# Optimization experiments

Hardware: AMD Instinct MI355X
Metric: run time of the kernel (lower is better)

Reference implementation:

```python
import jax, jax.numpy as jnp
import numpy as np

N = 4096
F = 1024
UNITS = 128
HEADS = 8
MASK_VAL = -10000000000.0  # -1e10, matches the source
LEAKY_ALPHA = 0.2


def setup_inputs() -> dict:
    key = jax.random.key(0)
    ks = jax.random.split(key, 6)
    X = jax.random.normal(ks[0], (1, N, F), dtype=jnp.float32)
    # Binary adjacency with self-loops (the layer expects self-loops preprocessed in).
    u = jax.random.uniform(ks[1], (N, N), dtype=jnp.float32)
    A = ((u < 0.01).astype(jnp.float32) + jnp.eye(N, dtype=jnp.float32))
    A = jnp.minimum(A, 1.0)[None]  # [1, N, N]
    W = jax.random.normal(ks[2], (HEADS, F, UNITS), dtype=jnp.float32) * (1.0 / np.sqrt(F))
    a_self = jax.random.normal(ks[3], (HEADS, UNITS), dtype=jnp.float32) * 0.1
    a_neigh = jax.random.normal(ks[4], (HEADS, UNITS), dtype=jnp.float32) * 0.1
    b = jnp.zeros((HEADS, UNITS), dtype=jnp.float32)
    return {"X": X, "A": A, "W": W, "a_self": a_self, "a_neigh": a_neigh, "b": b}


def reference(X, A, W, a_self, a_neigh, b):
    x = X[0]   # [N, F]
    adj = A[0]  # [N, N]
    # Per-head feature projection: [H, N, U]
    feat = jnp.einsum("nf,hfu->hnu", x, W)
    # Additive attention logits: e_ij = leaky_relu(a_s . h_i + a_n . h_j)
    s = jnp.einsum("hnu,hu->hn", feat, a_self)    # [H, N]
    t = jnp.einsum("hnu,hu->hn", feat, a_neigh)   # [H, N]
    dense = s[:, :, None] + t[:, None, :]          # [H, N, N]
    dense = jax.nn.leaky_relu(dense, negative_slope=LEAKY_ALPHA)
    # Mask non-edges with -1e10 (dense += -1e10 * (1 - A))
    dense = dense + MASK_VAL * (1.0 - adj)[None]
    attn = jax.nn.softmax(dense, axis=-1)          # [H, N, N]
    # Weighted aggregation + bias: [H, N, U]
    h = jnp.einsum("hnm,hmu->hnu", attn, feat) + b[:, None, :]
    # Concat heads: [N, H*U]
    out = jnp.transpose(h, (1, 0, 2)).reshape(N, HEADS * UNITS)
    out = jax.nn.relu(out)
    return out[None]  # [1, N, H*U]
```

## Files before the change

### kernel.cpp

```cpp
#include <hip/hip_runtime.h>


constexpr int NN = 4096;
constexpr int FF = 1024;
constexpr int HH = 8;
constexpr int UU = 128;
constexpr int CC = HH * UU;
constexpr int MAXDEG = 128;
constexpr float ALPHA = 0.2f;

typedef __attribute__((ext_vector_type(8))) short short8;
typedef __attribute__((ext_vector_type(4))) float f32x4;

__device__ inline unsigned short f2bf(float x) {
  unsigned u = __float_as_uint(x);
  return (unsigned short)((u + 0x7fffu + ((u >> 16) & 1u)) >> 16);
}
__device__ inline float bf2f(unsigned short h) { return __uint_as_float(((unsigned)h) << 16); }

__global__ __launch_bounds__(256) void transposeW(const float* __restrict__ W,
                                                  unsigned short* __restrict__ WT) {
  const int h = blockIdx.x >> 3, ft = blockIdx.x & 7;
  const int f0 = ft * 128;
  __shared__ unsigned short hiT[128][136];
  __shared__ unsigned short loT[128][136];
  const int tid = threadIdx.x;
#pragma unroll
  for (int it = 0; it < 16; ++it) {
    int idx = it * 256 + tid;
    int r = idx >> 5;
    int u4 = idx & 31;
    float4 v = *(const float4*)(W + (size_t)h * FF * UU + (size_t)(f0 + r) * UU + u4 * 4);
    float xs[4] = {v.x, v.y, v.z, v.w};
#pragma unroll
    for (int e = 0; e < 4; ++e) {
      unsigned short hb = f2bf(xs[e]);
      hiT[u4 * 4 + e][r] = hb;
      loT[u4 * 4 + e][r] = f2bf(xs[e] - bf2f(hb));
    }
  }
  __syncthreads();
#pragma unroll
  for (int it = 0; it < 8; ++it) {
    int idx = it * 256 + tid;
    int u = idx >> 4, f8 = idx & 15;
    short8 vh = *(const short8*)&hiT[u][f8 * 8];
    short8 vl = *(const short8*)&loT[u][f8 * 8];
    size_t o = (size_t)h * UU * FF + (size_t)u * FF + f0 + f8 * 8;
    *(short8*)(WT + o) = vh;
    *(short8*)(WT + (size_t)HH * UU * FF + o) = vl;
  }
}

__global__ __launch_bounds__(256) void prep(const float* __restrict__ X,
                                            unsigned short* __restrict__ Xhi,
                                            unsigned short* __restrict__ Xlo,
                                            const float* __restrict__ A,
                                            int* __restrict__ deg,
                                            int* __restrict__ idx) {
  const int tid = threadIdx.x;
  if (blockIdx.x < 2048) {
    size_t base = ((size_t)blockIdx.x * 256 + tid) * 8;
    float4 v0 = *(const float4*)(X + base);
    float4 v1 = *(const float4*)(X + base + 4);
    float xs[8] = {v0.x, v0.y, v0.z, v0.w, v1.x, v1.y, v1.z, v1.w};
    short8 vh, vl;
#pragma unroll
    for (int e = 0; e < 8; ++e) {
      unsigned short hb = f2bf(xs[e]);
      vh[e] = (short)hb;
      vl[e] = (short)f2bf(xs[e] - bf2f(hb));
    }
    *(short8*)(Xhi + base) = vh;
    *(short8*)(Xlo + base) = vl;
    return;
  }
  const int i = blockIdx.x - 2048;
  const int lane = tid & 63;
  __shared__ int cnt;
  if (tid == 0) cnt = 0;
  __syncthreads();
  const float4* row = reinterpret_cast<const float4*>(A + (size_t)i * NN);
  for (int c = tid; c < NN / 4; c += 256) {
    float4 v = row[c];
    unsigned long long m0 = __ballot(v.x > 0.5f);
    unsigned long long m1 = __ballot(v.y > 0.5f);
    unsigned long long m2 = __ballot(v.z > 0.5f);
    unsigned long long m3 = __ballot(v.w > 0.5f);
    int wtot = __popcll(m0) + __popcll(m1) + __popcll(m2) + __popcll(m3);
    if (wtot) {
      int base = 0;
      if (lane == 0) base = atomicAdd(&cnt, wtot);
      base = __shfl(base, 0);
      unsigned long long lt = (1ull << lane) - 1;
      int c0 = __popcll(m0), c1 = __popcll(m1), c2 = __popcll(m2);
      int o;
      o = base + __popcll(m0 & lt);
      if (v.x > 0.5f && o < MAXDEG) idx[i * MAXDEG + o] = c * 4 + 0;
      o = base + c0 + __popcll(m1 & lt);
      if (v.y > 0.5f && o < MAXDEG) idx[i * MAXDEG + o] = c * 4 + 1;
      o = base + c0 + c1 + __popcll(m2 & lt);
      if (v.z > 0.5f && o < MAXDEG) idx[i * MAXDEG + o] = c * 4 + 2;
      o = base + c0 + c1 + c2 + __popcll(m3 & lt);
      if (v.w > 0.5f && o < MAXDEG) idx[i * MAXDEG + o] = c * 4 + 3;
    }
  }
  __syncthreads();
  if (tid == 0) deg[i] = cnt > MAXDEG ? MAXDEG : cnt;
}

constexpr int NTILE = 48;

__global__ __launch_bounds__(512) void gemm_mfma(const unsigned short* __restrict__ Xhi,
                                                 const unsigned short* __restrict__ Xlo,
                                                 const unsigned short* __restrict__ WT,
                                                 const float* __restrict__ a_self,
                                                 const float* __restrict__ a_neigh,
                                                 float* __restrict__ featH,
                                                 float* __restrict__ s_arr,
                                                 float* __restrict__ t_arr) {
  __shared__ char lds[2][32768];
  const int tid = threadIdx.x;
  const int w = tid >> 6, l = tid & 63;
  const int h = blockIdx.x >> 5;
  const int row0 = (blockIdx.x & 31) * 128;
  const int wr = w >> 2, wc = w & 3;

  const int lr = l >> 3;
  const int sk = ((l & 7) ^ lr) * 8;
  const unsigned short* WTh = WT + (size_t)h * UU * FF;

  f32x4 acc[4][2] = {};

  auto stage = [&](int t, int buf) {
    int s = t >> 4, kt = t & 15;
    const unsigned short* As = ((s == 1) ? Xlo : Xhi) +
        (size_t)(row0 + w * 16 + lr) * FF + kt * 64 + sk;
    const unsigned short* Bs = WTh + ((s == 2) ? (size_t)HH * UU * FF : (size_t)0) +
        (size_t)(w * 16 + lr) * FF + kt * 64 + sk;
    char* la = &lds[buf][w * 2048];
    char* lb = &lds[buf][16384 + w * 2048];
#pragma unroll
    for (int dr = 0; dr < 2; ++dr) {
      __builtin_amdgcn_global_load_lds(
          (const __attribute__((address_space(1))) unsigned int*)(As + (size_t)dr * 8 * FF),
          (__attribute__((address_space(3))) unsigned int*)(la + dr * 1024), 16, 0, 0);
      __builtin_amdgcn_global_load_lds(
          (const __attribute__((address_space(1))) unsigned int*)(Bs + (size_t)dr * 8 * FF),
          (__attribute__((address_space(3))) unsigned int*)(lb + dr * 1024), 16, 0, 0);
    }
  };

  const int arow = wr * 64 + (l & 15);
  const int bcol = wc * 32 + (l & 15);
  const int kswz = (l & 7) << 4;
  const int kb = (l >> 4) * 16;

  auto compute = [&](int buf) {
#pragma unroll
    for (int ks = 0; ks < 2; ++ks) {
      const int ko = ks * 64 + kb;
      short8 a[4], b[2];
#pragma unroll
      for (int mi = 0; mi < 4; ++mi)
        a[mi] = *(const short8*)(&lds[buf][(arow + mi * 16) * 128 + (ko ^ kswz)]);
#pragma unroll
      for (int ni = 0; ni < 2; ++ni)
        b[ni] = *(const short8*)(&lds[buf][16384 + (bcol + ni * 16) * 128 + (ko ^ kswz)]);
#pragma unroll
      for (int mi = 0; mi < 4; ++mi)
#pragma unroll
        for (int ni = 0; ni < 2; ++ni)
          acc[mi][ni] = __builtin_amdgcn_mfma_f32_16x16x32_bf16(a[mi], b[ni],
                                                                acc[mi][ni], 0, 0, 0);
    }
  };

  stage(0, 0);
  __syncthreads();
  for (int tt = 0; tt < NTILE; ++tt) {
    if (tt + 1 < NTILE) stage(tt + 1, (tt + 1) & 1);
    compute(tt & 1);
    __syncthreads();
  }

  float* fh = featH + (size_t)h * NN * UU;
  const int cu = wc * 32 + (l & 15);
  const int crow0 = row0 + wr * 64 + (l >> 4) * 4;
#pragma unroll
  for (int mi = 0; mi < 4; ++mi)
#pragma unroll
    for (int ni = 0; ni < 2; ++ni)
#pragma unroll
      for (int r = 0; r < 4; ++r)
        fh[(size_t)(crow0 + mi * 16 + r) * UU + cu + ni * 16] = acc[mi][ni][r];

  const float as0 = a_self[h * UU + cu], as1 = a_self[h * UU + cu + 16];
  const float an0 = a_neigh[h * UU + cu], an1 = a_neigh[h * UU + cu + 16];
  float ps[16], pt[16];
#pragma unroll
  for (int mi = 0; mi < 4; ++mi)
#pragma unroll
    for (int r = 0; r < 4; ++r) {
      ps[mi * 4 + r] = acc[mi][0][r] * as0 + acc[mi][1][r] * as1;
      pt[mi * 4 + r] = acc[mi][0][r] * an0 + acc[mi][1][r] * an1;
    }
#pragma unroll
  for (int mask = 1; mask <= 8; mask <<= 1)
#pragma unroll
    for (int q = 0; q < 16; ++q) {
      ps[q] += __shfl_xor(ps[q], mask);
      pt[q] += __shfl_xor(pt[q], mask);
    }
  float(*sred)[4] = (float(*)[4]) & lds[0][0];
  float(*tred)[4] = (float(*)[4]) & lds[0][2048];
  if ((l & 15) == 0) {
#pragma unroll
    for (int mi = 0; mi < 4; ++mi)
#pragma unroll
      for (int r = 0; r < 4; ++r) {
        int rl = wr * 64 + mi * 16 + (l >> 4) * 4 + r;
        sred[rl][wc] = ps[mi * 4 + r];
        tred[rl][wc] = pt[mi * 4 + r];
      }
  }
  __syncthreads();
  if (tid < 128) {
    float sv = sred[tid][0] + sred[tid][1] + sred[tid][2] + sred[tid][3];
    float tv = tred[tid][0] + tred[tid][1] + tred[tid][2] + tred[tid][3];
    s_arr[h * NN + row0 + tid] = sv;
    t_arr[h * NN + row0 + tid] = tv;
  }
}

__global__ __launch_bounds__(256) void aggregate(const float* __restrict__ featH,
                                                 const float* __restrict__ s_arr,
                                                 const float* __restrict__ t_arr,
                                                 const int* __restrict__ deg_arr,
                                                 const int* __restrict__ idx_arr,
                                                 const float* __restrict__ bias,
                                                 float* __restrict__ out) {
  const int b = blockIdx.x;
  const int h = b >> 9;
  const int i = ((b & 511) << 3) + (threadIdx.x >> 5);
  const int s32 = threadIdx.x & 31;
  const int slot = threadIdx.x >> 5;
  __shared__ int jj[8][MAXDEG];
  __shared__ float p[8][MAXDEG];

  const int deg = deg_arr[i];
  const float si = s_arr[h * NN + i];
  float e[4];
#pragma unroll
  for (int c = 0; c < 4; ++c) {
    int k = s32 + c * 32;
    int j = (k < deg) ? idx_arr[i * MAXDEG + k] : 0;
    if (k < deg) jj[slot][k] = j;
    if (k < deg) {
      float x = si + t_arr[h * NN + j];
      e[c] = x > 0.0f ? x : ALPHA * x;
    } else {
      e[c] = -3e38f;
    }
  }
  float m = fmaxf(fmaxf(e[0], e[1]), fmaxf(e[2], e[3]));
#pragma unroll
  for (int mask = 1; mask <= 16; mask <<= 1) m = fmaxf(m, __shfl_xor(m, mask));
  float pv[4], sum = 0.0f;
#pragma unroll
  for (int c = 0; c < 4; ++c) {
    pv[c] = __expf(e[c] - m);
    sum += pv[c];
  }
#pragma unroll
  for (int mask = 1; mask <= 16; mask <<= 1) sum += __shfl_xor(sum, mask);
  const float inv = 1.0f / sum;
#pragma unroll
  for (int c = 0; c < 4; ++c) p[slot][s32 + c * 32] = pv[c];

  const float* fb = featH + (size_t)h * NN * UU + s32 * 4;
  float ax = 0.0f, ay = 0.0f, az = 0.0f, aw = 0.0f;
  int k = 0;
  for (; k + 3 < deg; k += 4) {
    int j0 = jj[slot][k], j1 = jj[slot][k + 1];
    int j2 = jj[slot][k + 2], j3 = jj[slot][k + 3];
    float p0 = p[slot][k], p1 = p[slot][k + 1];
    float p2 = p[slot][k + 2], p3 = p[slot][k + 3];
    float4 v0 = *(const float4*)(fb + (size_t)j0 * UU);
    float4 v1 = *(const float4*)(fb + (size_t)j1 * UU);
    float4 v2 = *(const float4*)(fb + (size_t)j2 * UU);
    float4 v3 = *(const float4*)(fb + (size_t)j3 * UU);
    ax += p0 * v0.x + p1 * v1.x + p2 * v2.x + p3 * v3.x;
    ay += p0 * v0.y + p1 * v1.y + p2 * v2.y + p3 * v3.y;
    az += p0 * v0.z + p1 * v1.z + p2 * v2.z + p3 * v3.z;
    aw += p0 * v0.w + p1 * v1.w + p2 * v2.w + p3 * v3.w;
  }
  for (; k < deg; ++k) {
    float pk = p[slot][k];
    float4 v = *(const float4*)(fb + (size_t)jj[slot][k] * UU);
    ax += pk * v.x; ay += pk * v.y; az += pk * v.z; aw += pk * v.w;
  }
  const float4 b4 = *(const float4*)(bias + h * UU + s32 * 4);
  float4 o;
  o.x = fmaxf(ax * inv + b4.x, 0.0f);
  o.y = fmaxf(ay * inv + b4.y, 0.0f);
  o.z = fmaxf(az * inv + b4.z, 0.0f);
  o.w = fmaxf(aw * inv + b4.w, 0.0f);
  *(float4*)(out + (size_t)i * CC + h * UU + s32 * 4) = o;
}

extern "C" void kernel_launch(void* const* d_in, const int* in_sizes, int n_in,
                              void* d_out, int out_size, void* d_ws, size_t ws_size,
                              hipStream_t stream) {
  const float* X       = (const float*)d_in[0];
  const float* A       = (const float*)d_in[1];
  const float* W       = (const float*)d_in[2];
  const float* a_self  = (const float*)d_in[3];
  const float* a_neigh = (const float*)d_in[4];
  const float* bias    = (const float*)d_in[5];
  float* out = (float*)d_out;

  float* featH = (float*)d_ws;
  unsigned short* Xhi = (unsigned short*)(featH + (size_t)NN * CC);
  unsigned short* Xlo = Xhi + (size_t)NN * FF;
  unsigned short* WT  = Xlo + (size_t)NN * FF;
  float* s_arr = (float*)(WT + (size_t)2 * HH * UU * FF);
  float* t_arr = s_arr + HH * NN;
  int* deg = (int*)(t_arr + HH * NN);
  int* idx = deg + NN;

  hipLaunchKernelGGL(transposeW, dim3(64), dim3(256), 0, stream, W, WT);
  hipLaunchKernelGGL(prep, dim3(2048 + NN), dim3(256), 0, stream,
                     X, Xhi, Xlo, A, deg, idx);
  hipLaunchKernelGGL(gemm_mfma, dim3(256), dim3(512), 0, stream,
                     Xhi, Xlo, WT, a_self, a_neigh, featH, s_arr, t_arr);
  hipLaunchKernelGGL(aggregate, dim3(NN), dim3(256), 0, stream,
                     featH, s_arr, t_arr, deg, idx, bias, out);
}
```

Baseline: 207.4 us.

## Split GEMM K-loop in two halves and reduce partial sums

The projection GEMM now runs 512 blocks, each covering half of the 48 K tiles (split-K), and writes its partial features and s/t scores into one of two workspace buffers. A new reduce_add kernel sums the two partials into the final feature and score arrays. The goal is to double the block count so the 256-CU device is better filled, at the cost of writing, rereading and summing about 32 MB of fp32 partials plus one more kernel launch.

Result: slower. 214.7 us (+3.5%).

```diff
diff --git a/kernel.cpp b/kernel.cpp
--- a/kernel.cpp
+++ b/kernel.cpp
@@ -8,6 +8,9 @@
 constexpr int CC = HH * UU;
 constexpr int MAXDEG = 128;
 constexpr float ALPHA = 0.2f;
+constexpr size_t FEAT_ELEMS = (size_t)NN * CC;
+constexpr size_t ST_ELEMS = (size_t)HH * NN;
+constexpr size_t OUTBLK = FEAT_ELEMS + 2 * ST_ELEMS;
 
 typedef __attribute__((ext_vector_type(8))) short short8;
 typedef __attribute__((ext_vector_type(4))) float f32x4;
@@ -109,22 +112,27 @@
   if (tid == 0) deg[i] = cnt > MAXDEG ? MAXDEG : cnt;
 }
 
-constexpr int NTILE = 48;
-
 __global__ __launch_bounds__(512) void gemm_mfma(const unsigned short* __restrict__ Xhi,
                                                  const unsigned short* __restrict__ Xlo,
                                                  const unsigned short* __restrict__ WT,
                                                  const float* __restrict__ a_self,
                                                  const float* __restrict__ a_neigh,
-                                                 float* __restrict__ featH,
-                                                 float* __restrict__ s_arr,
-                                                 float* __restrict__ t_arr) {
+                                                 float* __restrict__ pA,
+                                                 float* __restrict__ pB) {
   __shared__ char lds[2][32768];
   const int tid = threadIdx.x;
   const int w = tid >> 6, l = tid & 63;
-  const int h = blockIdx.x >> 5;
-  const int row0 = (blockIdx.x & 31) * 128;
+  const int bid = blockIdx.x;
+  const int z = bid >> 8;
+  const int bid8 = bid & 255;
+  const int h = bid8 >> 5;
+  const int row0 = (bid8 & 31) * 128;
   const int wr = w >> 2, wc = w & 3;
+  const int t0 = z * 24;
+
+  float* pf = z ? pB : pA;
+  float* ps = pf + FEAT_ELEMS;
+  float* pt = ps + ST_ELEMS;
 
   const int lr = l >> 3;
   const int sk = ((l & 7) ^ lr) * 8;
@@ -176,15 +184,15 @@
     }
   };
 
-  stage(0, 0);
-  __syncthreads();
-  for (int tt = 0; tt < NTILE; ++tt) {
-    if (tt + 1 < NTILE) stage(tt + 1, (tt + 1) & 1);
+  stage(t0, 0);
+  __syncthreads();
+  for (int tt = 0; tt < 24; ++tt) {
+    if (tt + 1 < 24) stage(t0 + tt + 1, (tt + 1) & 1);
     compute(tt & 1);
     __syncthreads();
   }
 
-  float* fh = featH + (size_t)h * NN * UU;
+  float* fh = pf + (size_t)h * NN * UU;
   const int cu = wc * 32 + (l & 15);
   const int crow0 = row0 + wr * 64 + (l >> 4) * 4;
 #pragma unroll
@@ -197,20 +205,20 @@
 
   const float as0 = a_self[h * UU + cu], as1 = a_self[h * UU + cu + 16];
   const float an0 = a_neigh[h * UU + cu], an1 = a_neigh[h * UU + cu + 16];
-  float ps[16], pt[16];
+  float psr[16], ptr_[16];
 #pragma unroll
   for (int mi = 0; mi < 4; ++mi)
 #pragma unroll
     for (int r = 0; r < 4; ++r) {
-      ps[mi * 4 + r] = acc[mi][0][r] * as0 + acc[mi][1][r] * as1;
-      pt[mi * 4 + r] = acc[mi][0][r] * an0 + acc[mi][1][r] * an1;
+      psr[mi * 4 + r] = acc[mi][0][r] * as0 + acc[mi][1][r] * as1;
+      ptr_[mi * 4 + r] = acc[mi][0][r] * an0 + acc[mi][1][r] * an1;
     }
 #pragma unroll
   for (int mask = 1; mask <= 8; mask <<= 1)
 #pragma unroll
     for (int q = 0; q < 16; ++q) {
-      ps[q] += __shfl_xor(ps[q], mask);
-      pt[q] += __shfl_xor(pt[q], mask);
+      psr[q] += __shfl_xor(psr[q], mask);
+      ptr_[q] += __shfl_xor(ptr_[q], mask);
     }
   float(*sred)[4] = (float(*)[4]) & lds[0][0];
   float(*tred)[4] = (float(*)[4]) & lds[0][2048];
@@ -220,16 +228,29 @@
 #pragma unroll
       for (int r = 0; r < 4; ++r) {
         int rl = wr * 64 + mi * 16 + (l >> 4) * 4 + r;
-        sred[rl][wc] = ps[mi * 4 + r];
-        tred[rl][wc] = pt[mi * 4 + r];
+        sred[rl][wc] = psr[mi * 4 + r];
+        tred[rl][wc] = ptr_[mi * 4 + r];
       }
   }
   __syncthreads();
   if (tid < 128) {
     float sv = sred[tid][0] + sred[tid][1] + sred[tid][2] + sred[tid][3];
     float tv = tred[tid][0] + tred[tid][1] + tred[tid][2] + tred[tid][3];
-    s_arr[h * NN + row0 + tid] = sv;
-    t_arr[h * NN + row0 + tid] = tv;
+    ps[h * NN + row0 + tid] = sv;
+    pt[h * NN + row0 + tid] = tv;
+  }
+}
+
+__global__ __launch_bounds__(256) void reduce_add(const float* __restrict__ pA,
+                                                  const float* __restrict__ pB,
+                                                  float* __restrict__ outw) {
+  size_t base = ((size_t)blockIdx.x * 256 + threadIdx.x) * 16;
+#pragma unroll
+  for (int q = 0; q < 4; ++q) {
+    float4 a = *(const float4*)(pA + base + q * 4);
+    float4 b = *(const float4*)(pB + base + q * 4);
+    float4 o = make_float4(a.x + b.x, a.y + b.y, a.z + b.z, a.w + b.w);
+    *(float4*)(outw + base + q * 4) = o;
   }
 }
 
@@ -321,19 +342,22 @@
   float* out = (float*)d_out;
 
   float* featH = (float*)d_ws;
-  unsigned short* Xhi = (unsigned short*)(featH + (size_t)NN * CC);
+  float* s_arr = featH + FEAT_ELEMS;
+  float* t_arr = s_arr + ST_ELEMS;
+  float* pA = featH + OUTBLK;
+  float* pB = pA + OUTBLK;
+  unsigned short* Xhi = (unsigned short*)(pB + OUTBLK);
   unsigned short* Xlo = Xhi + (size_t)NN * FF;
   unsigned short* WT  = Xlo + (size_t)NN * FF;
-  float* s_arr = (float*)(WT + (size_t)2 * HH * UU * FF);
-  float* t_arr = s_arr + HH * NN;
-  int* deg = (int*)(t_arr + HH * NN);
+  int* deg = (int*)(WT + (size_t)2 * HH * UU * FF);
   int* idx = deg + NN;
 
   hipLaunchKernelGGL(transposeW, dim3(64), dim3(256), 0, stream, W, WT);
   hipLaunchKernelGGL(prep, dim3(2048 + NN), dim3(256), 0, stream,
                      X, Xhi, Xlo, A, deg, idx);
-  hipLaunchKernelGGL(gemm_mfma, dim3(256), dim3(512), 0, stream,
-                     Xhi, Xlo, WT, a_self, a_neigh, featH, s_arr, t_arr);
+  hipLaunchKernelGGL(gemm_mfma, dim3(512), dim3(512), 0, stream,
+                     Xhi, Xlo, WT, a_self, a_neigh, pA, pB);
+  hipLaunchKernelGGL(reduce_add, dim3(1040), dim3(256), 0, stream, pA, pB, featH);
   hipLaunchKernelGGL(aggregate, dim3(NN), dim3(256), 0, stream,
                      featH, s_arr, t_arr, deg, idx, bias, out);
 }
```
